# Kernel optimization log

Measured on AMD Instinct MI355X. Metric: run time of the kernel, lower is better.

Reference implementation:

```python
import jax, jax.numpy as jnp
import numpy as np

P_DROP = 0.25
DROP_KEY_SEED = 42  # fixed seed makes dropout deterministic for baseline comparison


def setup_inputs() -> dict:
    key = jax.random.key(0)
    k1, k2, k3, k4 = jax.random.split(key, 4)
    B, S, D, DV = 16, 2048, 64, 512
    x1 = jax.random.normal(k1, (B, S, D), dtype=jnp.float32)   # queries [B,S,64]
    m = jax.random.normal(k2, (D, DV), dtype=jnp.float32)      # [64,512]
    n = jax.random.normal(k3, (S, DV), dtype=jnp.float32)      # [S,512]
    q = jax.random.normal(k4, (S, DV), dtype=jnp.float32)      # values [S,512]
    return {"x1": x1, "m": m, "n": n, "q": q}


def reference(x1, m, n, q):
    scale = jnp.float32(1.0 / 64.0)  # hard-coded in original (not 1/sqrt(d))
    kT = jnp.matmul(m, n.T)                        # matmul5: [64, S]
    scores = jnp.matmul(x1, kT) * scale            # [B, S, S]
    probs = jax.nn.softmax(scores, axis=-1)        # softmax over last dim
    keep = jax.random.bernoulli(jax.random.key(DROP_KEY_SEED), 1.0 - P_DROP, probs.shape)
    probs = jnp.where(keep, probs / (1.0 - P_DROP), jnp.float32(0.0))  # dropout (train mode)
    return jnp.matmul(probs, q)                    # [B, S, DV]
```

## Files before the change

kernel.cpp:

```cpp
#include <hip/hip_runtime.h>


typedef short  s8v __attribute__((ext_vector_type(8)));
typedef float  f4v __attribute__((ext_vector_type(4)));

__device__ __forceinline__ unsigned short f2bf(float f) {
  unsigned int u = __float_as_uint(f);
  u += 0x7fffu + ((u >> 16) & 1u);
  return (unsigned short)(u >> 16);
}
__device__ __forceinline__ float bf2f(unsigned short h) {
  return __uint_as_float(((unsigned int)h) << 16);
}

__device__ __forceinline__ unsigned int rotl(unsigned int x, unsigned int r) {
  return __builtin_amdgcn_alignbit(x, x, 32u - r);
}

__device__ __forceinline__ unsigned int jax_bits(unsigned int idx) {
  const unsigned int K0 = 0u, K1 = 42u, K2 = 0x1BD11BDAu ^ K0 ^ K1;
  unsigned int x0 = 0u, x1 = idx;
  x0 += K0; x1 += K1;
#define TF_R(r) { x0 += x1; x1 = rotl(x1, r); x1 ^= x0; }
  TF_R(13) TF_R(15) TF_R(26) TF_R(6)
  x0 += K1; x1 += K2 + 1u;
  TF_R(17) TF_R(29) TF_R(16) TF_R(24)
  x0 += K2; x1 += K0 + 2u;
  TF_R(13) TF_R(15) TF_R(26) TF_R(6)
  x0 += K0; x1 += K1 + 3u;
  TF_R(17) TF_R(29) TF_R(16) TF_R(24)
  x0 += K1; x1 += K2 + 4u;
  TF_R(13) TF_R(15) TF_R(26) TF_R(6)
  x0 += K2; x1 += K0 + 5u;
#undef TF_R
  return x0 ^ x1;
}

__device__ __forceinline__ f4v mfma16(s8v a, s8v b, f4v c) {
  return __builtin_amdgcn_mfma_f32_16x16x32_bf16(a, b, c, 0, 0, 0);
}

__global__ void prep_all(const float* __restrict__ x1, const float* __restrict__ q,
                         const float* __restrict__ m, const float* __restrict__ nmat,
                         unsigned short* __restrict__ Xhi, unsigned short* __restrict__ qT,
                         unsigned short* __restrict__ Khi, unsigned short* __restrict__ Klo) {
  const int blk = blockIdx.x;
  const int t = threadIdx.x;
  if (blk < 512) {
    __shared__ float Lm[64][68];
    const int s = blk * 4 + (t >> 6);
    const int d = t & 63;
    float a0 = 0.f, a1 = 0.f, a2 = 0.f, a3 = 0.f;
    for (int ch = 0; ch < 8; ++ch) {
      const int dv0 = ch * 64;
      __syncthreads();
#pragma unroll
      for (int k = 0; k < 4; ++k) {
        const int fi = t + k * 256;
        const int row = fi >> 4, c4 = fi & 15;
        *(float4*)&Lm[row][c4 * 4] =
            *(const float4*)&m[(size_t)row * 512 + dv0 + c4 * 4];
      }
      __syncthreads();
      const float4* nv = (const float4*)&nmat[(size_t)s * 512 + dv0];
#pragma unroll
      for (int j4 = 0; j4 < 16; ++j4) {
        const float4 nf = nv[j4];
        const float4 mf = *(const float4*)&Lm[d][j4 * 4];
        a0 = fmaf(mf.x, nf.x, a0); a1 = fmaf(mf.y, nf.y, a1);
        a2 = fmaf(mf.z, nf.z, a2); a3 = fmaf(mf.w, nf.w, a3);
      }
    }
    const float kv = ((a0 + a1) + (a2 + a3)) * (1.44269504088896340736f / 64.0f);
    const unsigned short h = f2bf(kv);
    Khi[s * 64 + d] = h;
    Klo[s * 64 + d] = f2bf(kv - bf2f(h));
  } else if (blk < 1536) {
    const int i = ((blk - 512) * 256 + t) * 8;
    float4 a = *(const float4*)&x1[i];
    float4 b = *(const float4*)&x1[i + 4];
    ushort4 o0, o1;
    o0.x = f2bf(a.x); o0.y = f2bf(a.y); o0.z = f2bf(a.z); o0.w = f2bf(a.w);
    o1.x = f2bf(b.x); o1.y = f2bf(b.y); o1.z = f2bf(b.z); o1.w = f2bf(b.w);
    *(ushort4*)&Xhi[i] = o0;
    *(ushort4*)&Xhi[i + 4] = o1;
  } else {
    __shared__ unsigned short tile[64][65];
    const int bb = blk - 1536;
    const int s0 = (bb >> 3) * 64;
    const int d0 = (bb & 7) * 64;
#pragma unroll
    for (int k = 0; k < 16; ++k) {
      int lin = t + k * 256;
      int r = lin >> 6, c = lin & 63;
      tile[c][r] = f2bf(q[(size_t)(s0 + r) * 512 + d0 + c]);
    }
    __syncthreads();
#pragma unroll
    for (int k = 0; k < 16; ++k) {
      int lin = t + k * 256;
      int rr = lin >> 6, cc = lin & 63;
      qT[(size_t)(d0 + rr) * 2048 + s0 + cc] = tile[rr][cc];
    }
  }
}

__global__ __launch_bounds__(512, 4) void attn_main(
    const unsigned short* __restrict__ Xhi,
    const unsigned short* __restrict__ Khi, const unsigned short* __restrict__ Klo,
    const unsigned short* __restrict__ qT, float* __restrict__ out) {
  __shared__ unsigned short Ps[2][64][136];
  __shared__ float rsum[2][64];

  const int tid  = threadIdx.x;
  const int wave = tid >> 6;
  const int lane = tid & 63;
  const int l15  = lane & 15;
  const int quad = lane >> 4;

  const int b    = blockIdx.x >> 5;
  const int row0 = (blockIdx.x & 31) * 64;

  const int qk_row = (wave & 3) * 16 + l15;
  const int qk_kg  = (wave >> 2) * 64;

  const size_t xg = ((size_t)(b * 2048 + row0 + qk_row)) * 64 + quad * 8;
  const s8v X0 = *(const s8v*)&Xhi[xg];
  const s8v X1 = *(const s8v*)&Xhi[xg + 32];

  f4v acc[4][4];
#pragma unroll
  for (int mt = 0; mt < 4; ++mt)
#pragma unroll
    for (int nt = 0; nt < 4; ++nt) acc[mt][nt] = f4v{0.f, 0.f, 0.f, 0.f};
  float rs = 0.f;

  const unsigned int idx_row =
      ((unsigned int)(b * 2048 + row0 + qk_row)) * 2048u;

  const unsigned short* __restrict__ khp = Khi + ((qk_kg + l15) * 64 + quad * 8);
  const unsigned short* __restrict__ klp = Klo + ((qk_kg + l15) * 64 + quad * 8);
  const unsigned short* __restrict__ qvp = qT + ((wave * 64 + l15) * 2048 + quad * 8);

  for (int it = 0; it < 16; ++it) {
    const int kt = it * 128;
    unsigned short (*Pb)[136] = Ps[it & 1];

#pragma unroll
    for (int nt = 0; nt < 4; ++nt) {
      const int ko = (kt + nt * 16) * 64;
      s8v Kh0 = *(const s8v*)(khp + ko);
      s8v Kh1 = *(const s8v*)(khp + ko + 32);
      s8v Kl0 = *(const s8v*)(klp + ko);
      s8v Kl1 = *(const s8v*)(klp + ko + 32);
      f4v c = {0.f, 0.f, 0.f, 0.f};
      c = mfma16(Kh0, X0, c);  c = mfma16(Kh1, X1, c);
      c = mfma16(Kl0, X0, c);  c = mfma16(Kl1, X1, c);
      const unsigned int idx0 = idx_row + (unsigned int)(kt + qk_kg + nt * 16 + quad * 4);
      float p[4];
#pragma unroll
      for (int r = 0; r < 4; ++r) {
        float e = exp2f(c[r]);
        rs += e;
        const unsigned int bits = jax_bits(idx0 + r);
        p[r] = (bits < 0xC0000000u) ? e : 0.0f;
      }
      unsigned int p01, p23;
      asm("v_cvt_pk_bf16_f32 %0, %1, %2" : "=v"(p01) : "v"(p[0]), "v"(p[1]));
      asm("v_cvt_pk_bf16_f32 %0, %1, %2" : "=v"(p23) : "v"(p[2]), "v"(p[3]));
      *(uint2*)&Pb[(wave & 3) * 16 + l15][qk_kg + nt * 16 + quad * 4] =
          make_uint2(p01, p23);
    }
    __syncthreads();

#pragma unroll
    for (int ks = 0; ks < 4; ++ks) {
      s8v Va[4];
#pragma unroll
      for (int mt = 0; mt < 4; ++mt)
        Va[mt] = *(const s8v*)(qvp + mt * (16 * 2048) + kt + ks * 32);
      __builtin_amdgcn_s_setprio(1);
#pragma unroll
      for (int nt = 0; nt < 4; ++nt) {
        s8v Pf = *(const s8v*)&Pb[nt * 16 + l15][ks * 32 + quad * 8];
#pragma unroll
        for (int mt = 0; mt < 4; ++mt) acc[mt][nt] = mfma16(Va[mt], Pf, acc[mt][nt]);
      }
      __builtin_amdgcn_s_setprio(0);
    }
  }

  {
    float v = rs;
    v += __shfl_xor(v, 16);
    v += __shfl_xor(v, 32);
    if (quad == 0) rsum[wave >> 2][(wave & 3) * 16 + l15] = v;
  }
  __syncthreads();

#pragma unroll
  for (int nt = 0; nt < 4; ++nt) {
    const int rloc = nt * 16 + l15;
    const int row = row0 + rloc;
    const float inv = 1.0f / (0.75f * (rsum[0][rloc] + rsum[1][rloc]));
    const size_t base = ((size_t)(b * 2048 + row)) * 512 + wave * 64;
#pragma unroll
    for (int mt = 0; mt < 4; ++mt) {
      f4v v = acc[mt][nt];
      v[0] *= inv; v[1] *= inv; v[2] *= inv; v[3] *= inv;
      *(f4v*)&out[base + mt * 16 + quad * 4] = v;
    }
  }
}

extern "C" void kernel_launch(void* const* d_in, const int* in_sizes, int n_in,
                              void* d_out, int out_size, void* d_ws, size_t ws_size,
                              hipStream_t stream) {
  (void)in_sizes; (void)n_in; (void)out_size; (void)ws_size;
  const float* x1 = (const float*)d_in[0];
  const float* m  = (const float*)d_in[1];
  const float* n  = (const float*)d_in[2];
  const float* q  = (const float*)d_in[3];
  float* out = (float*)d_out;

  char* ws = (char*)d_ws;
  unsigned short* Khi = (unsigned short*)(ws);
  unsigned short* Klo = (unsigned short*)(ws + 262144);
  unsigned short* Xhi = (unsigned short*)(ws + 524288);
  unsigned short* qT  = (unsigned short*)(ws + 4718592);

  prep_all<<<1792, 256, 0, stream>>>(x1, q, m, n, Xhi, qT, Khi, Klo);
  attn_main<<<512, 512, 0, stream>>>(Xhi, Khi, Klo, qT, out);
}
```

Baseline: 353.7 us.

## Swap QK work split so each wave keeps one K tile and reads X from LDS

Changes the QK^T work split so that each wave owns 16 key columns across all 64 query rows, rather than 16 query rows across 64 key columns. The X tile is staged once into shared memory, and the wave's K hi/lo fragments sit in registers. The next iteration's K fragments are prefetched before the barrier. This cuts global K loads per iteration from sixteen to four per lane and hides their latency, at the cost of LDS reads for X and an 8-way row-sum reduction through shared memory.

Result: faster. 312.3 us (-11.7%).

```diff
diff --git a/kernel.cpp b/kernel.cpp
--- a/kernel.cpp
+++ b/kernel.cpp
@@ -109,8 +109,9 @@
     const unsigned short* __restrict__ Xhi,
     const unsigned short* __restrict__ Khi, const unsigned short* __restrict__ Klo,
     const unsigned short* __restrict__ qT, float* __restrict__ out) {
+  __shared__ unsigned short Xs[64][72];
   __shared__ unsigned short Ps[2][64][136];
-  __shared__ float rsum[2][64];
+  __shared__ float rsum[8][64];
 
   const int tid  = threadIdx.x;
   const int wave = tid >> 6;
@@ -121,26 +122,33 @@
   const int b    = blockIdx.x >> 5;
   const int row0 = (blockIdx.x & 31) * 64;
 
-  const int qk_row = (wave & 3) * 16 + l15;
-  const int qk_kg  = (wave >> 2) * 64;
-
-  const size_t xg = ((size_t)(b * 2048 + row0 + qk_row)) * 64 + quad * 8;
-  const s8v X0 = *(const s8v*)&Xhi[xg];
-  const s8v X1 = *(const s8v*)&Xhi[xg + 32];
+  {
+    const int r = tid >> 3, c8 = (tid & 7) * 8;
+    *(uint4*)&Xs[r][c8] =
+        *(const uint4*)&Xhi[((size_t)(b * 2048 + row0 + r)) * 64 + c8];
+  }
+
+  const unsigned short* __restrict__ khp = Khi + ((wave * 16 + l15) * 64 + quad * 8);
+  const unsigned short* __restrict__ klp = Klo + ((wave * 16 + l15) * 64 + quad * 8);
+  const unsigned short* __restrict__ qvp = qT + ((wave * 64 + l15) * 2048 + quad * 8);
+
+  s8v Kh0 = *(const s8v*)(khp);
+  s8v Kh1 = *(const s8v*)(khp + 32);
+  s8v Kl0 = *(const s8v*)(klp);
+  s8v Kl1 = *(const s8v*)(klp + 32);
 
   f4v acc[4][4];
 #pragma unroll
   for (int mt = 0; mt < 4; ++mt)
 #pragma unroll
     for (int nt = 0; nt < 4; ++nt) acc[mt][nt] = f4v{0.f, 0.f, 0.f, 0.f};
-  float rs = 0.f;
-
-  const unsigned int idx_row =
-      ((unsigned int)(b * 2048 + row0 + qk_row)) * 2048u;
-
-  const unsigned short* __restrict__ khp = Khi + ((qk_kg + l15) * 64 + quad * 8);
-  const unsigned short* __restrict__ klp = Klo + ((qk_kg + l15) * 64 + quad * 8);
-  const unsigned short* __restrict__ qvp = qT + ((wave * 64 + l15) * 2048 + quad * 8);
+  float rs[4] = {0.f, 0.f, 0.f, 0.f};
+
+  const unsigned int idxl =
+      ((unsigned int)(b * 2048 + row0 + l15)) * 2048u +
+      (unsigned int)(wave * 16 + quad * 4);
+
+  __syncthreads();
 
   for (int it = 0; it < 16; ++it) {
     const int kt = it * 128;
@@ -148,29 +156,34 @@
 
 #pragma unroll
     for (int nt = 0; nt < 4; ++nt) {
-      const int ko = (kt + nt * 16) * 64;
-      s8v Kh0 = *(const s8v*)(khp + ko);
-      s8v Kh1 = *(const s8v*)(khp + ko + 32);
-      s8v Kl0 = *(const s8v*)(klp + ko);
-      s8v Kl1 = *(const s8v*)(klp + ko + 32);
+      const s8v Xb0 = *(const s8v*)&Xs[nt * 16 + l15][quad * 8];
+      const s8v Xb1 = *(const s8v*)&Xs[nt * 16 + l15][quad * 8 + 32];
       f4v c = {0.f, 0.f, 0.f, 0.f};
-      c = mfma16(Kh0, X0, c);  c = mfma16(Kh1, X1, c);
-      c = mfma16(Kl0, X0, c);  c = mfma16(Kl1, X1, c);
-      const unsigned int idx0 = idx_row + (unsigned int)(kt + qk_kg + nt * 16 + quad * 4);
+      c = mfma16(Kh0, Xb0, c);  c = mfma16(Kh1, Xb1, c);
+      c = mfma16(Kl0, Xb0, c);  c = mfma16(Kl1, Xb1, c);
+      const unsigned int idx0 = idxl + (unsigned int)(nt * 32768 + kt);
       float p[4];
 #pragma unroll
       for (int r = 0; r < 4; ++r) {
         float e = exp2f(c[r]);
-        rs += e;
+        rs[nt] += e;
         const unsigned int bits = jax_bits(idx0 + r);
         p[r] = (bits < 0xC0000000u) ? e : 0.0f;
       }
       unsigned int p01, p23;
       asm("v_cvt_pk_bf16_f32 %0, %1, %2" : "=v"(p01) : "v"(p[0]), "v"(p[1]));
       asm("v_cvt_pk_bf16_f32 %0, %1, %2" : "=v"(p23) : "v"(p[2]), "v"(p[3]));
-      *(uint2*)&Pb[(wave & 3) * 16 + l15][qk_kg + nt * 16 + quad * 4] =
-          make_uint2(p01, p23);
-    }
+      *(uint2*)&Pb[nt * 16 + l15][wave * 16 + quad * 4] = make_uint2(p01, p23);
+    }
+
+    if (it < 15) {
+      const int ko = (it + 1) * 8192;
+      Kh0 = *(const s8v*)(khp + ko);
+      Kh1 = *(const s8v*)(khp + ko + 32);
+      Kl0 = *(const s8v*)(klp + ko);
+      Kl1 = *(const s8v*)(klp + ko + 32);
+    }
+
     __syncthreads();
 
 #pragma unroll
@@ -182,7 +195,7 @@
       __builtin_amdgcn_s_setprio(1);
 #pragma unroll
       for (int nt = 0; nt < 4; ++nt) {
-        s8v Pf = *(const s8v*)&Pb[nt * 16 + l15][ks * 32 + quad * 8];
+        const s8v Pf = *(const s8v*)&Pb[nt * 16 + l15][ks * 32 + quad * 8];
 #pragma unroll
         for (int mt = 0; mt < 4; ++mt) acc[mt][nt] = mfma16(Va[mt], Pf, acc[mt][nt]);
       }
@@ -190,20 +203,23 @@
     }
   }
 
-  {
-    float v = rs;
+#pragma unroll
+  for (int nt = 0; nt < 4; ++nt) {
+    float v = rs[nt];
     v += __shfl_xor(v, 16);
     v += __shfl_xor(v, 32);
-    if (quad == 0) rsum[wave >> 2][(wave & 3) * 16 + l15] = v;
+    if (quad == 0) rsum[wave][nt * 16 + l15] = v;
   }
   __syncthreads();
 
 #pragma unroll
   for (int nt = 0; nt < 4; ++nt) {
     const int rloc = nt * 16 + l15;
-    const int row = row0 + rloc;
-    const float inv = 1.0f / (0.75f * (rsum[0][rloc] + rsum[1][rloc]));
-    const size_t base = ((size_t)(b * 2048 + row)) * 512 + wave * 64;
+    float tot = 0.f;
+#pragma unroll
+    for (int w2 = 0; w2 < 8; ++w2) tot += rsum[w2][rloc];
+    const float inv = 1.0f / (0.75f * tot);
+    const size_t base = ((size_t)(b * 2048 + row0 + rloc)) * 512 + wave * 64;
 #pragma unroll
     for (int mt = 0; mt < 4; ++mt) {
       f4v v = acc[mt][nt];
```
